# Kernel tuning notes

Measured on AMD Instinct MI355X. Metric: run time of the kernel, lower is better.

## Reference

```python
import jax, jax.numpy as jnp
import numpy as np

NUM_HEADS = 4
NUM_GROUPS = 8
EPS = 1e-5


def group_norm(x, w, b):
    # x: (B, C, H, W); normalize per group of C//NUM_GROUPS channels
    B, C, H, W = x.shape
    xg = x.reshape(B, NUM_GROUPS, C // NUM_GROUPS, H, W)
    mean = xg.mean(axis=(2, 3, 4), keepdims=True)
    var = xg.var(axis=(2, 3, 4), keepdims=True)
    xn = ((xg - mean) * jax.lax.rsqrt(var + EPS)).reshape(B, C, H, W)
    return xn * w[None, :, None, None] + b[None, :, None, None]


def conv1x1(x, w, b):
    # x: (B, C_in, H, W), w: (C_out, C_in), b: (C_out,)
    return jnp.einsum('bchw,oc->bohw', x, w) + b[None, :, None, None]


def setup_inputs() -> dict:
    key = jax.random.key(0)
    B, C, H, W = 4, 256, 64, 64
    k1, k2, k3 = jax.random.split(key, 3)
    scale = 1.0 / np.sqrt(C)
    return {
        'x': jax.random.normal(k1, (B, C, H, W), dtype=jnp.float32),
        'norm_w': jnp.ones((C,), dtype=jnp.float32),
        'norm_b': jnp.zeros((C,), dtype=jnp.float32),
        'qkv_w': jax.random.normal(k2, (3 * C, C), dtype=jnp.float32) * scale,
        'qkv_b': jnp.zeros((3 * C,), dtype=jnp.float32),
        'proj_w': jax.random.normal(k3, (C, C), dtype=jnp.float32) * scale,
        'proj_b': jnp.zeros((C,), dtype=jnp.float32),
    }


def reference(x, norm_w, norm_b, qkv_w, qkv_b, proj_w, proj_b):
    B, C, H, W = x.shape
    hd = C // NUM_HEADS  # head dim
    h = group_norm(x, norm_w, norm_b)
    qkv = conv1x1(h, qkv_w, qkv_b)            # (B, 3C, H, W)
    q, k, v = jnp.split(qkv, 3, axis=1)
    q = q.reshape(B, NUM_HEADS, hd, H * W)
    k = k.reshape(B, NUM_HEADS, hd, H * W)
    v = v.reshape(B, NUM_HEADS, hd, H * W)
    attn = jnp.einsum('bhcn,bhcm->bhnm', q, k) / jnp.sqrt(jnp.asarray(hd, x.dtype))
    attn = jax.nn.softmax(attn, axis=-1)
    out = jnp.einsum('bhnm,bhcm->bhcn', attn, v).reshape(B, C, H, W)
    out = conv1x1(out, proj_w, proj_b)
    return x + out
```

## Files before the change

kernel.cpp:

```cpp
#include <hip/hip_runtime.h>
#include <hip/hip_bf16.h>
#include <stdint.h>


#define B_  4
#define C_  256
#define N_  4096
#define NH_ 4
#define HD_ 64
#define G_  8
#define CPG_ 32
#define GRP_ELEMS (CPG_ * N_)

typedef __attribute__((ext_vector_type(8))) short short8;
typedef __attribute__((ext_vector_type(4))) float f32x4;
typedef __attribute__((ext_vector_type(4))) unsigned short us4;

__device__ __forceinline__ unsigned short f2bf(float f) {
  union { float f; unsigned u; } v; v.f = f;
  unsigned r = v.u + 0x7FFFu + ((v.u >> 16) & 1u);
  return (unsigned short)(r >> 16);
}

__device__ __forceinline__ unsigned pkbf2(float a, float b) {
  __hip_bfloat162 h = __float22bfloat162_rn(make_float2(a, b));
  unsigned r; __builtin_memcpy(&r, &h, sizeof(r)); return r;
}

__device__ __forceinline__ void dma16(const unsigned short* g, unsigned short* l) {
  __builtin_amdgcn_global_load_lds(
      (const __attribute__((address_space(1))) unsigned int*)(g),
      (__attribute__((address_space(3))) unsigned int*)(l), 16, 0, 0);
}

__global__ void gn_partial_cvt(const float* __restrict__ x, float* __restrict__ partial,
                               const float* __restrict__ qkvw, const float* __restrict__ projw,
                               unsigned short* __restrict__ wq, unsigned short* __restrict__ wp) {
  __shared__ float ls[8];
  int t = threadIdx.x;
  if (blockIdx.x >= 512) {
    int i = (blockIdx.x - 512) * 256 + t;
    if (i < 768 * 256) wq[i] = f2bf(qkvw[i]);
    if (i < 256 * 256) wp[i] = f2bf(projw[i]);
    return;
  }
  int idx = blockIdx.x;
  int slice = idx & 15, g = (idx >> 4) & 7, b = idx >> 7;
  const float* base = x + (size_t)(b * C_ + g * CPG_) * N_ + slice * 256;
  float s = 0.f, sq = 0.f;
#pragma unroll
  for (int cc = 0; cc < CPG_; cc++) {
    float v = base[(size_t)cc * N_ + t];
    s += v; sq += v * v;
  }
#pragma unroll
  for (int off = 32; off; off >>= 1) {
    s  += __shfl_down(s,  off, 64);
    sq += __shfl_down(sq, off, 64);
  }
  int wave = t >> 6, lane = t & 63;
  if (lane == 0) { ls[wave * 2] = s; ls[wave * 2 + 1] = sq; }
  __syncthreads();
  if (t == 0) {
    float S = ls[0] + ls[2] + ls[4] + ls[6];
    float SQ = ls[1] + ls[3] + ls[5] + ls[7];
    partial[idx * 2] = S; partial[idx * 2 + 1] = SQ;
  }
}

__global__ void gn_apply(const float* __restrict__ x,
                         const float* __restrict__ nw, const float* __restrict__ nb,
                         const float* __restrict__ partial, unsigned short* __restrict__ hT) {
  int nt = blockIdx.x, ct = blockIdx.y, b = blockIdx.z;
  __shared__ unsigned short tile[32][72];
  int t = threadIdx.x;
  int lane = t & 63;
  int grp = b * G_ + ct;
  float s = 0.f, sq = 0.f;
  if (lane < 16) {
    s  = partial[(grp * 16 + lane) * 2];
    sq = partial[(grp * 16 + lane) * 2 + 1];
  }
#pragma unroll
  for (int off = 8; off; off >>= 1) {
    s  += __shfl_down(s,  off, 64);
    sq += __shfl_down(sq, off, 64);
  }
  s  = __shfl(s,  0, 64);
  sq = __shfl(sq, 0, 64);
  const float inv = 1.0f / (float)GRP_ELEMS;
  float mean = s * inv;
  float rstd = rsqrtf(sq * inv - mean * mean + 1e-5f);

  int n_loc = t & 63, c_loc = t >> 6;
  const float* xb = x + (size_t)(b * C_ + ct * CPG_) * N_ + nt * 64;
#pragma unroll
  for (int rr = 0; rr < 8; rr++) {
    int cc = rr * 4 + c_loc;
    int c = ct * CPG_ + cc;
    float v = xb[(size_t)cc * N_ + n_loc];
    v = (v - mean) * rstd * nw[c] + nb[c];
    tile[cc][n_loc] = f2bf(v);
  }
  __syncthreads();
  int n = t >> 2, c8 = (t & 3) * 8;
  us4 lo, hi;
#pragma unroll
  for (int j = 0; j < 4; j++) lo[j] = tile[c8 + j][n];
#pragma unroll
  for (int j = 0; j < 4; j++) hi[j] = tile[c8 + 4 + j][n];
  unsigned short* outp = hT + ((size_t)(b * N_ + nt * 64 + n)) * C_ + ct * CPG_ + c8;
  *reinterpret_cast<us4*>(outp) = lo;
  *reinterpret_cast<us4*>(outp + 4) = hi;
}

__global__ __launch_bounds__(256) void qkv_gemm(
    const unsigned short* __restrict__ hT, const unsigned short* __restrict__ wq,
    const float* __restrict__ qb,
    unsigned short* __restrict__ Qt, unsigned short* __restrict__ Kt,
    unsigned short* __restrict__ V) {
  int ot = blockIdx.x >> 7;
  int nt = (blockIdx.x & 127) >> 2;
  int b  = blockIdx.x & 3;
  int t = threadIdx.x;
  int wave = t >> 6, lane = t & 63, l15 = lane & 15, quad = lane >> 4, l7 = l15 & 7;

  __shared__ __align__(16) unsigned short sh[128 * C_];
  {
    int row0 = wave * 2 + (lane >> 5);
    int col8 = lane & 31;
    int src8 = (col8 & 24) | ((col8 & 7) ^ (row0 & 7));
    const unsigned short* gsrc = hT + ((size_t)(b * N_ + nt * 128 + row0)) * C_ + src8 * 8;
#pragma unroll
    for (int it = 0; it < 16; it++)
      dma16(gsrc + (size_t)it * 8 * C_, sh + (it * 8 + wave * 2) * C_);
  }

  f32x4 acc[2][8];
#pragma unroll
  for (int r = 0; r < 2; r++)
#pragma unroll
    for (int tt = 0; tt < 8; tt++) acc[r][tt] = (f32x4){0.f, 0.f, 0.f, 0.f};

  const short8* arow[2];
#pragma unroll
  for (int r = 0; r < 2; r++)
    arow[r] = reinterpret_cast<const short8*>(
        wq + (size_t)(ot * 128 + wave * 32 + r * 16 + l15) * C_);

  asm volatile("s_waitcnt vmcnt(0)" ::: "memory");
  __syncthreads();

#pragma unroll
  for (int kk = 0; kk < 8; kk++) {
    int g = kk * 4 + quad;
    int col8 = (g & 24) | ((g & 7) ^ l7);
    short8 bfr[8];
#pragma unroll
    for (int tt = 0; tt < 8; tt++)
      bfr[tt] = *reinterpret_cast<const short8*>(&sh[(tt * 16 + l15) * C_ + col8 * 8]);
#pragma unroll
    for (int r = 0; r < 2; r++) {
      short8 a = arow[r][g];
#pragma unroll
      for (int tt = 0; tt < 8; tt++)
        acc[r][tt] = __builtin_amdgcn_mfma_f32_16x16x32_bf16(a, bfr[tt], acc[r][tt], 0, 0, 0);
    }
  }

  int sec = ot >> 1;
  int head = (ot & 1) * 2 + (wave >> 1);
  int bh = b * NH_ + head;
  const float SC = 0.125f * 1.44269504088896340736f;

#pragma unroll
  for (int r = 0; r < 2; r++) {
    int o_glob = ot * 128 + wave * 32 + r * 16;
    int cw = (o_glob & 63) + quad * 4;
    if (sec == 0) {
#pragma unroll
      for (int tt = 0; tt < 8; tt++) {
        int n = nt * 128 + tt * 16 + l15;
        us4 pk;
#pragma unroll
        for (int i = 0; i < 4; i++)
          pk[i] = f2bf((acc[r][tt][i] + qb[o_glob + quad * 4 + i]) * SC);
        *reinterpret_cast<us4*>(Qt + ((size_t)bh * N_ + n) * HD_ + cw) = pk;
      }
    } else if (sec == 1) {
#pragma unroll
      for (int tt = 0; tt < 8; tt++) {
        int n = nt * 128 + tt * 16 + l15;
        us4 pk;
#pragma unroll
        for (int i = 0; i < 4; i++)
          pk[i] = f2bf(acc[r][tt][i] + qb[o_glob + quad * 4 + i]);
        *reinterpret_cast<us4*>(Kt + ((size_t)bh * N_ + n) * HD_ + cw) = pk;
      }
    } else {
#pragma unroll
      for (int tt = 0; tt < 8; tt++) {
        int n = nt * 128 + tt * 16 + l15;
#pragma unroll
        for (int i = 0; i < 4; i++)
          V[((size_t)bh * HD_ + cw + i) * N_ + n] =
              f2bf(acc[r][tt][i] + qb[o_glob + quad * 4 + i]);
      }
    }
  }
}

__global__ __launch_bounds__(256, 2) void flash_attn(
    const unsigned short* __restrict__ Qt, const unsigned short* __restrict__ Kt,
    const unsigned short* __restrict__ Vv, unsigned short* __restrict__ aoT) {
  int bh = blockIdx.x & 15, qt = blockIdx.x >> 4;
  int b = bh >> 2, head = bh & 3;
  int t = threadIdx.x;
  int wave = t >> 6, lane = t & 63, l15 = lane & 15, quad = lane >> 4;
  int l7 = l15 & 7;

  const unsigned short* Qb = Qt + (size_t)bh * N_ * HD_;
  const unsigned short* Kb = Kt + (size_t)bh * N_ * HD_;
  const unsigned short* Vb = Vv + (size_t)bh * HD_ * N_;
  int q_base = qt * 128 + wave * 32;

  __shared__ __align__(16) unsigned short KV[2][2][4096];

  const short8 vones = {(short)0x3F80, (short)0x3F80, (short)0x3F80, (short)0x3F80,
                        (short)0x3F80, (short)0x3F80, (short)0x3F80, (short)0x3F80};
  const f32x4 fzero = (f32x4){0.f, 0.f, 0.f, 0.f};

  short8 qf[2][2];
#pragma unroll
  for (int r = 0; r < 2; r++)
#pragma unroll
    for (int h = 0; h < 2; h++)
      qf[r][h] = *reinterpret_cast<const short8*>(
          Qb + (size_t)(q_base + r * 16 + l15) * HD_ + h * 32 + quad * 8);

  f32x4 oa[2][4], la[2];
#pragma unroll
  for (int r = 0; r < 2; r++) {
    la[r] = (f32x4){0.f, 0.f, 0.f, 0.f};
#pragma unroll
    for (int ct = 0; ct < 4; ct++) oa[r][ct] = (f32x4){0.f, 0.f, 0.f, 0.f};
  }

  int i8 = lane >> 3, e = lane & 7;
  int perm = (e ^ i8) * 8;
  auto stage = [&](int kt2, int buf) {
    int m0 = kt2 * 64;
    unsigned short* Kd = &KV[0][buf][0];
    unsigned short* Vd = &KV[1][buf][0];
#pragma unroll
    for (int cc = 0; cc < 2; cc++) {
      int c = wave * 2 + cc;
      dma16(Kb + (size_t)(m0 + c * 8 + i8) * HD_ + perm, Kd + c * 512);
      dma16(Vb + (size_t)(c * 8 + i8) * N_ + m0 + perm, Vd + c * 512);
    }
  };

  stage(0, 0);

#pragma unroll 1
  for (int kt = 0; kt < 64; kt++) {
    int buf = kt & 1;
    if (kt + 1 < 64) {
      stage(kt + 1, buf ^ 1);
      asm volatile("s_waitcnt vmcnt(4)" ::: "memory");
    } else {
      asm volatile("s_waitcnt vmcnt(0)" ::: "memory");
    }
    __builtin_amdgcn_s_barrier();

    const unsigned short* Kbuf = &KV[0][buf][0];
    const unsigned short* Vbuf = &KV[1][buf][0];

    short8 kf[4][2], vf[4][2];
#pragma unroll
    for (int tt = 0; tt < 4; tt++)
#pragma unroll
      for (int kh2 = 0; kh2 < 2; kh2++) {
        kf[tt][kh2] = *reinterpret_cast<const short8*>(
            &Kbuf[(tt * 16 + l15) * 64 + (((kh2 * 4 + quad) ^ l7) * 8)]);
        vf[tt][kh2] = *reinterpret_cast<const short8*>(
            &Vbuf[(tt * 16 + l15) * 64 + (((kh2 * 4 + quad) ^ l7) * 8)]);
      }

#pragma unroll
    for (int r = 0; r < 2; r++) {
      f32x4 s[4];
#pragma unroll
      for (int tt = 0; tt < 4; tt++) {
        f32x4 z = __builtin_amdgcn_mfma_f32_16x16x32_bf16(kf[tt][0], qf[r][0], fzero, 0, 0, 0);
        s[tt] = __builtin_amdgcn_mfma_f32_16x16x32_bf16(kf[tt][1], qf[r][1], z, 0, 0, 0);
      }
      unsigned Apk[4], Bpk[4];
#pragma unroll
      for (int tt = 0; tt < 4; tt++) {
        Apk[tt] = pkbf2(__builtin_amdgcn_exp2f(s[tt][0]), __builtin_amdgcn_exp2f(s[tt][1]));
        Bpk[tt] = pkbf2(__builtin_amdgcn_exp2f(s[tt][2]), __builtin_amdgcn_exp2f(s[tt][3]));
      }
      union { unsigned u[4]; short8 v; } f0, f1;
      {
        auto ua = __builtin_amdgcn_permlane32_swap(Apk[0], Apk[1], false, false);
        auto pa = __builtin_amdgcn_permlane16_swap(ua[0], ua[1], false, false);
        auto ub = __builtin_amdgcn_permlane32_swap(Bpk[0], Bpk[1], false, false);
        auto pb = __builtin_amdgcn_permlane16_swap(ub[0], ub[1], false, false);
        f0.u[0] = pa[0]; f0.u[1] = pb[0]; f0.u[2] = pa[1]; f0.u[3] = pb[1];
        auto uc = __builtin_amdgcn_permlane32_swap(Apk[2], Apk[3], false, false);
        auto pc = __builtin_amdgcn_permlane16_swap(uc[0], uc[1], false, false);
        auto ud = __builtin_amdgcn_permlane32_swap(Bpk[2], Bpk[3], false, false);
        auto pd = __builtin_amdgcn_permlane16_swap(ud[0], ud[1], false, false);
        f1.u[0] = pc[0]; f1.u[1] = pd[0]; f1.u[2] = pc[1]; f1.u[3] = pd[1];
      }
      short8 pf0 = f0.v, pf1 = f1.v;
#pragma unroll
      for (int ct = 0; ct < 4; ct++) {
        oa[r][ct] = __builtin_amdgcn_mfma_f32_16x16x32_bf16(vf[ct][0], pf0, oa[r][ct], 0, 0, 0);
        oa[r][ct] = __builtin_amdgcn_mfma_f32_16x16x32_bf16(vf[ct][1], pf1, oa[r][ct], 0, 0, 0);
      }
      la[r] = __builtin_amdgcn_mfma_f32_16x16x32_bf16(vones, pf0, la[r], 0, 0, 0);
      la[r] = __builtin_amdgcn_mfma_f32_16x16x32_bf16(vones, pf1, la[r], 0, 0, 0);
    }
  }

#pragma unroll
  for (int r = 0; r < 2; r++) {
    float inv = 1.0f / la[r][0];
    int n = q_base + r * 16 + l15;
#pragma unroll
    for (int ct = 0; ct < 4; ct++) {
      union { unsigned u2[2]; us4 v; } w;
      w.u2[0] = pkbf2(oa[r][ct][0] * inv, oa[r][ct][1] * inv);
      w.u2[1] = pkbf2(oa[r][ct][2] * inv, oa[r][ct][3] * inv);
      *reinterpret_cast<us4*>(
          aoT + ((size_t)(b * N_ + n)) * C_ + head * HD_ + ct * 16 + quad * 4) = w.v;
    }
  }
}

__global__ __launch_bounds__(256) void proj_gemm(
    const unsigned short* __restrict__ aoT, const unsigned short* __restrict__ wp,
    const float* __restrict__ pb, const float* __restrict__ x,
    float* __restrict__ out) {
  int ot = blockIdx.x >> 7;
  int nt = (blockIdx.x & 127) >> 2;
  int b  = blockIdx.x & 3;
  int t = threadIdx.x;
  int wave = t >> 6, lane = t & 63, l15 = lane & 15, quad = lane >> 4, l7 = l15 & 7;
  int o_base = ot * 64 + wave * 16;

  __shared__ __align__(16) unsigned short sh[128 * C_];
  {
    int row0 = wave * 2 + (lane >> 5);
    int col8 = lane & 31;
    int src8 = (col8 & 24) | ((col8 & 7) ^ (row0 & 7));
    const unsigned short* gsrc = aoT + ((size_t)(b * N_ + nt * 128 + row0)) * C_ + src8 * 8;
#pragma unroll
    for (int it = 0; it < 16; it++)
      dma16(gsrc + (size_t)it * 8 * C_, sh + (it * 8 + wave * 2) * C_);
  }

  f32x4 acc[8];
#pragma unroll
  for (int tt = 0; tt < 8; tt++) acc[tt] = (f32x4){0.f, 0.f, 0.f, 0.f};

  const short8* arow = reinterpret_cast<const short8*>(wp + (size_t)(o_base + l15) * C_);

  asm volatile("s_waitcnt vmcnt(0)" ::: "memory");
  __syncthreads();

#pragma unroll
  for (int kk = 0; kk < 8; kk++) {
    short8 a = arow[kk * 4 + quad];
    int g = kk * 4 + quad;
    int col8 = (g & 24) | ((g & 7) ^ l7);
#pragma unroll
    for (int tt = 0; tt < 8; tt++) {
      short8 bf = *reinterpret_cast<const short8*>(&sh[(tt * 16 + l15) * C_ + col8 * 8]);
      acc[tt] = __builtin_amdgcn_mfma_f32_16x16x32_bf16(a, bf, acc[tt], 0, 0, 0);
    }
  }
#pragma unroll
  for (int tt = 0; tt < 8; tt++) {
    int n = nt * 128 + tt * 16 + l15;
#pragma unroll
    for (int i = 0; i < 4; i++) {
      int o = o_base + quad * 4 + i;
      size_t idx = ((size_t)(b * C_ + o)) * N_ + n;
      out[idx] = acc[tt][i] + pb[o] + x[idx];
    }
  }
}

extern "C" void kernel_launch(void* const* d_in, const int* in_sizes, int n_in,
                              void* d_out, int out_size, void* d_ws, size_t ws_size,
                              hipStream_t stream) {
  const float* x      = (const float*)d_in[0];
  const float* norm_w = (const float*)d_in[1];
  const float* norm_b = (const float*)d_in[2];
  const float* qkv_w  = (const float*)d_in[3];
  const float* qkv_b  = (const float*)d_in[4];
  const float* proj_w = (const float*)d_in[5];
  const float* proj_b = (const float*)d_in[6];
  float* out = (float*)d_out;

  char* ws = (char*)d_ws;
  size_t off = 0;
  auto alloc = [&](size_t bytes) { size_t o = off; off = (off + bytes + 255) & ~(size_t)255; return o; };
  size_t off_partial = alloc(512 * 2 * sizeof(float));
  size_t off_stats   = alloc(32 * 2 * sizeof(float));
  size_t off_wq      = alloc((size_t)768 * 256 * 2);
  size_t off_wp      = alloc((size_t)256 * 256 * 2);
  size_t off_hT      = alloc((size_t)B_ * N_ * C_ * 2);
  size_t off_Qt      = alloc((size_t)B_ * NH_ * N_ * HD_ * 2);
  size_t off_Kt      = alloc((size_t)B_ * NH_ * N_ * HD_ * 2);
  size_t off_V       = alloc((size_t)B_ * NH_ * HD_ * N_ * 2);
  size_t off_aoT     = alloc((size_t)B_ * N_ * C_ * 2);
  (void)off_stats;

  float* partial = (float*)(ws + off_partial);
  unsigned short* wq  = (unsigned short*)(ws + off_wq);
  unsigned short* wp  = (unsigned short*)(ws + off_wp);
  unsigned short* hT  = (unsigned short*)(ws + off_hT);
  unsigned short* Qt  = (unsigned short*)(ws + off_Qt);
  unsigned short* Kt  = (unsigned short*)(ws + off_Kt);
  unsigned short* V   = (unsigned short*)(ws + off_V);
  unsigned short* aoT = (unsigned short*)(ws + off_aoT);

  gn_partial_cvt<<<1280, 256, 0, stream>>>(x, partial, qkv_w, proj_w, wq, wp);
  gn_apply<<<dim3(64, 8, 4), 256, 0, stream>>>(x, norm_w, norm_b, partial, hT);
  qkv_gemm<<<768, 256, 0, stream>>>(hT, wq, qkv_b, Qt, Kt, V);
  flash_attn<<<512, 256, 0, stream>>>(Qt, Kt, V, aoT);
  proj_gemm<<<512, 256, 0, stream>>>(aoT, wp, proj_b, x, out);
}
```

Baseline: 188.0 us.

## Split flash attention over two key halves and merge partial outputs

The attention kernel now splits the key/value sequence into two halves, so twice as many blocks each do half the key loop. Each block writes unnormalized fp32 partial outputs and row sums to workspace, and a new merge kernel adds the two partials, normalizes them and writes the bf16 attention output. The aim is more parallelism and better latency hiding across the GPU's compute units. In exchange it adds tens of megabytes of fp32 intermediate writes and reads plus an extra kernel launch. The merge relies on the attention kernel applying no per-split running-max rescaling.

```diff
diff --git a/kernel.cpp b/kernel.cpp
--- a/kernel.cpp
+++ b/kernel.cpp
@@ -212,8 +212,9 @@
 
 __global__ __launch_bounds__(256, 2) void flash_attn(
     const unsigned short* __restrict__ Qt, const unsigned short* __restrict__ Kt,
-    const unsigned short* __restrict__ Vv, unsigned short* __restrict__ aoT) {
-  int bh = blockIdx.x & 15, qt = blockIdx.x >> 4;
+    const unsigned short* __restrict__ Vv, float* __restrict__ Opart,
+    float* __restrict__ lpart) {
+  int bh = blockIdx.x & 15, qt = (blockIdx.x >> 4) & 31, ks = blockIdx.x >> 9;
   int b = bh >> 2, head = bh & 3;
   int t = threadIdx.x;
   int wave = t >> 6, lane = t & 63, l15 = lane & 15, quad = lane >> 4;
@@ -223,6 +224,7 @@
   const unsigned short* Kb = Kt + (size_t)bh * N_ * HD_;
   const unsigned short* Vb = Vv + (size_t)bh * HD_ * N_;
   int q_base = qt * 128 + wave * 32;
+  int k_base = ks * 2048;
 
   __shared__ __align__(16) unsigned short KV[2][2][4096];
 
@@ -249,7 +251,7 @@
   int i8 = lane >> 3, e = lane & 7;
   int perm = (e ^ i8) * 8;
   auto stage = [&](int kt2, int buf) {
-    int m0 = kt2 * 64;
+    int m0 = k_base + kt2 * 64;
     unsigned short* Kd = &KV[0][buf][0];
     unsigned short* Vd = &KV[1][buf][0];
 #pragma unroll
@@ -263,9 +265,9 @@
   stage(0, 0);
 
 #pragma unroll 1
-  for (int kt = 0; kt < 64; kt++) {
+  for (int kt = 0; kt < 32; kt++) {
     int buf = kt & 1;
-    if (kt + 1 < 64) {
+    if (kt + 1 < 32) {
       stage(kt + 1, buf ^ 1);
       asm volatile("s_waitcnt vmcnt(4)" ::: "memory");
     } else {
@@ -325,19 +327,36 @@
     }
   }
 
+  float* Od = Opart + (size_t)ks * B_ * N_ * C_;
 #pragma unroll
   for (int r = 0; r < 2; r++) {
-    float inv = 1.0f / la[r][0];
     int n = q_base + r * 16 + l15;
 #pragma unroll
-    for (int ct = 0; ct < 4; ct++) {
-      union { unsigned u2[2]; us4 v; } w;
-      w.u2[0] = pkbf2(oa[r][ct][0] * inv, oa[r][ct][1] * inv);
-      w.u2[1] = pkbf2(oa[r][ct][2] * inv, oa[r][ct][3] * inv);
-      *reinterpret_cast<us4*>(
-          aoT + ((size_t)(b * N_ + n)) * C_ + head * HD_ + ct * 16 + quad * 4) = w.v;
-    }
-  }
+    for (int ct = 0; ct < 4; ct++)
+      *reinterpret_cast<f32x4*>(
+          Od + ((size_t)(b * N_ + n)) * C_ + head * HD_ + ct * 16 + quad * 4) = oa[r][ct];
+    if (quad == 0) lpart[(size_t)(ks * 16 + bh) * N_ + n] = la[r][0];
+  }
+}
+
+__global__ __launch_bounds__(256) void attn_merge(
+    const float* __restrict__ Opart, const float* __restrict__ lpart,
+    unsigned short* __restrict__ aoT) {
+  int g = blockIdx.x * 256 + threadIdx.x;
+  int c4 = g & 63;
+  int n  = (g >> 6) & (N_ - 1);
+  int b  = g >> 18;
+  int head = c4 >> 4;
+  int bh = b * NH_ + head;
+  size_t base = ((size_t)(b * N_ + n)) * C_ + c4 * 4;
+  f32x4 p0 = *reinterpret_cast<const f32x4*>(Opart + base);
+  f32x4 p1 = *reinterpret_cast<const f32x4*>(Opart + (size_t)B_ * N_ * C_ + base);
+  float inv = 1.0f / (lpart[(size_t)bh * N_ + n] +
+                      lpart[(size_t)(B_ * NH_ + bh) * N_ + n]);
+  union { unsigned u2[2]; us4 v; } w;
+  w.u2[0] = pkbf2((p0[0] + p1[0]) * inv, (p0[1] + p1[1]) * inv);
+  w.u2[1] = pkbf2((p0[2] + p1[2]) * inv, (p0[3] + p1[3]) * inv);
+  *reinterpret_cast<us4*>(aoT + base) = w.v;
 }
 
 __global__ __launch_bounds__(256) void proj_gemm(
@@ -418,6 +437,8 @@
   size_t off_Kt      = alloc((size_t)B_ * NH_ * N_ * HD_ * 2);
   size_t off_V       = alloc((size_t)B_ * NH_ * HD_ * N_ * 2);
   size_t off_aoT     = alloc((size_t)B_ * N_ * C_ * 2);
+  size_t off_Opart   = alloc((size_t)2 * B_ * N_ * C_ * 4);
+  size_t off_lpart   = alloc((size_t)2 * B_ * NH_ * N_ * 4);
   (void)off_stats;
 
   float* partial = (float*)(ws + off_partial);
@@ -428,10 +449,13 @@
   unsigned short* Kt  = (unsigned short*)(ws + off_Kt);
   unsigned short* V   = (unsigned short*)(ws + off_V);
   unsigned short* aoT = (unsigned short*)(ws + off_aoT);
+  float* Opart = (float*)(ws + off_Opart);
+  float* lpart = (float*)(ws + off_lpart);
 
   gn_partial_cvt<<<1280, 256, 0, stream>>>(x, partial, qkv_w, proj_w, wq, wp);
   gn_apply<<<dim3(64, 8, 4), 256, 0, stream>>>(x, norm_w, norm_b, partial, hT);
   qkv_gemm<<<768, 256, 0, stream>>>(hT, wq, qkv_b, Qt, Kt, V);
-  flash_attn<<<512, 256, 0, stream>>>(Qt, Kt, V, aoT);
+  flash_attn<<<1024, 256, 0, stream>>>(Qt, Kt, V, Opart, lpart);
+  attn_merge<<<4096, 256, 0, stream>>>(Opart, lpart, aoT);
   proj_gemm<<<512, 256, 0, stream>>>(aoT, wp, proj_b, x, out);
 }
```

Measured after the change: 194.3 us. 1.03x slower.
